# Optimization experiments

Hardware: AMD Instinct MI355X
Metric: run time of the kernel (lower is better)

The kernel has to match this reference:

```python
import jax, jax.numpy as jnp
import numpy as np

N_NODES = 20000
N_REL = 200
DIM = 128
N_EDGES = 200000
N_TIMES = 8


def setup_inputs() -> dict:
    key = jax.random.key(0)
    ks = jax.random.split(key, 12)
    s = 1.0 / np.sqrt(DIM)
    return {
        "edge_index": jax.random.randint(ks[0], (2, N_EDGES), 0, N_NODES),
        "edge_type": jax.random.randint(ks[1], (N_EDGES,), 0, N_REL),
        "edge_time": jax.random.randint(ks[2], (N_EDGES,), 0, N_TIMES),
        "edge_weight": jax.random.uniform(ks[3], (N_EDGES,), dtype=jnp.float32),
        "node_emb": jax.random.normal(ks[4], (N_NODES, DIM), dtype=jnp.float32),
        "rel_emb": jax.random.normal(ks[5], (N_REL, DIM), dtype=jnp.float32),
        "W_enc": jax.random.normal(ks[6], (DIM, DIM), dtype=jnp.float32) * s,
        "Wz": jax.random.normal(ks[7], (DIM, DIM), dtype=jnp.float32) * s,
        "Uz": jax.random.normal(ks[8], (DIM, DIM), dtype=jnp.float32) * s,
        "Wh": jax.random.normal(ks[9], (DIM, DIM), dtype=jnp.float32) * s,
        "Uh": jax.random.normal(ks[10], (DIM, DIM), dtype=jnp.float32) * s,
        "bz": jnp.zeros((DIM,), dtype=jnp.float32),
        "bh": jnp.zeros((DIM,), dtype=jnp.float32),
        "num_times": N_TIMES,
    }


def reference(edge_index, edge_type, edge_time, edge_weight,
              node_emb, rel_emb, W_enc, Wz, Uz, Wh, Uh, bz, bh, num_times):
    # TemporalEncoder.forward: loop over sorted unique timestamps; per-step
    # masked-edge GNN encode (R-GCN lite) then gated SSM cell; state detached.
    src, dst = edge_index[0], edge_index[1]
    rel_e = rel_emb[edge_type]          # [E, D] gather (constant across steps)
    src_e = node_emb[src]               # [E, D]
    n_nodes = node_emb.shape[0]

    def step(state, t):
        m = (edge_time == t).astype(edge_weight.dtype)       # [E]
        msg = src_e * rel_e * (edge_weight * m)[:, None]     # [E, D]
        agg = jax.ops.segment_sum(msg, dst, num_segments=n_nodes)  # [N, D]
        h = jnp.tanh(agg @ W_enc)                            # base_encoder output
        z = jax.nn.sigmoid(h @ Wz + state @ Uz + bz)
        cand = jnp.tanh(h @ Wh + state @ Uh + bh)
        new_state = (1.0 - z) * state + z * cand             # ssm.cell
        return jax.lax.stop_gradient(new_state), new_state   # state.detach()

    state0 = jnp.zeros_like(node_emb)
    _, outs = jax.lax.scan(step, state0, jnp.arange(num_times))
    return outs[-1]  # last_out, shape [N, D]
```

## Files before the change

### kernel.cpp

```cpp
#include <hip/hip_runtime.h>

#define N_NODES 20000
#define N_REL 200
#define N_EDGES 200000
#define DIM 128
#define T_STEPS 8
#define N_TILES (N_NODES / 16)
#define KEYS (N_NODES * T_STEPS)
#define SCAN_N (KEYS + 1)
#define SCAN_BLKS ((SCAN_N + 1023) / 1024)

typedef short short8 __attribute__((ext_vector_type(8)));
typedef float f32x4 __attribute__((ext_vector_type(4)));

static __device__ __forceinline__ unsigned short f2bf(float f) {
  union { float f; unsigned u; } v; v.f = f;
  unsigned r = v.u + 0x7fffu + ((v.u >> 16) & 1u);
  return (unsigned short)(r >> 16);
}
static __device__ __forceinline__ unsigned cvt_pk_bf16(float lo, float hi) {
  unsigned r;
  asm("v_cvt_pk_bf16_f32 %0, %1, %2" : "=v"(r) : "v"(lo), "v"(hi));
  return r;
}
static __device__ __forceinline__ float fast_tanh(float x) {
  float e = __expf(2.f * x);
  return 1.f - 2.f / (e + 1.f);
}
static __device__ __forceinline__ float fast_sig(float x) {
  return 1.f / (1.f + __expf(-x));
}

__global__ void repack5(const float* __restrict__ w0,
                        const float* __restrict__ w1,
                        const float* __restrict__ w2,
                        const float* __restrict__ w3,
                        const float* __restrict__ w4,
                        unsigned short* __restrict__ pack) {
  int i = blockIdx.x * blockDim.x + threadIdx.x;
  if (i >= 5 * 16384) return;
  int m = i >> 14, r = i & 16383;
  int j = r & 7, lane = (r >> 3) & 63, ks = (r >> 9) & 3, nt = (r >> 11) & 7;
  int n = nt * 16 + (lane & 15);
  int k = ks * 32 + (lane >> 4) * 8 + j;
  const float* w = (m == 0) ? w0 : (m == 1) ? w1 : (m == 2) ? w2
                 : (m == 3) ? w3 : w4;
  pack[i] = f2bf(w[k * DIM + n]);
}

__global__ void hist_k(const int* __restrict__ dst, const int* __restrict__ etime,
                       int* __restrict__ counts) {
  int i = blockIdx.x * blockDim.x + threadIdx.x;
  if (i >= N_EDGES) return;
  atomicAdd(&counts[dst[i] * T_STEPS + etime[i]], 1);
}

__global__ void scan1_k(const int* __restrict__ counts,
                        int* __restrict__ base, int* __restrict__ bsum) {
  __shared__ int ls[256];
  int tid = threadIdx.x;
  int i0 = blockIdx.x * 1024 + tid * 4;
  int v[4], ts = 0;
#pragma unroll
  for (int r = 0; r < 4; r++) {
    v[r] = (i0 + r < SCAN_N) ? counts[i0 + r] : 0;
    ts += v[r];
  }
  ls[tid] = ts; __syncthreads();
#pragma unroll
  for (int off = 1; off < 256; off <<= 1) {
    int x = (tid >= off) ? ls[tid - off] : 0;
    __syncthreads(); ls[tid] += x; __syncthreads();
  }
  int run = ls[tid] - ts;
  if (tid == 255) bsum[blockIdx.x] = ls[255];
#pragma unroll
  for (int r = 0; r < 4; r++) {
    if (i0 + r < SCAN_N) base[i0 + r] = run;
    run += v[r];
  }
}

__global__ void scan2_k(int* __restrict__ bsum) {
  __shared__ int ls[256];
  int tid = threadIdx.x;
  int v = (tid < SCAN_BLKS) ? bsum[tid] : 0;
  ls[tid] = v; __syncthreads();
#pragma unroll
  for (int off = 1; off < 256; off <<= 1) {
    int x = (tid >= off) ? ls[tid - off] : 0;
    __syncthreads(); ls[tid] += x; __syncthreads();
  }
  if (tid < SCAN_BLKS) bsum[tid] = ls[tid] - v;
}

__global__ void fill_k(const int* __restrict__ src, const int* __restrict__ dst,
                       const int* __restrict__ etype, const int* __restrict__ etime,
                       const float* __restrict__ ew,
                       const int* __restrict__ base, const int* __restrict__ bsum,
                       int* __restrict__ cursor, uint2* __restrict__ ep2) {
  int i = blockIdx.x * blockDim.x + threadIdx.x;
  if (i >= N_EDGES) return;
  int key = dst[i] * T_STEPS + etime[i];
  int pos = base[key] + bsum[key >> 10] + atomicAdd(&cursor[key], 1);
  uint2 e;
  e.x = (unsigned)src[i] | ((unsigned)etype[i] << 15);
  e.y = __float_as_uint(ew[i]);
  ep2[pos] = e;
}

__launch_bounds__(512, 4)
__global__ void fused_recur(const int* __restrict__ base,
                            const int* __restrict__ bsum,
                            const uint2* __restrict__ ep2,
                            const float* __restrict__ nemb,
                            const float* __restrict__ remb,
                            const unsigned short* __restrict__ pack,
                            const float* __restrict__ bz,
                            const float* __restrict__ bh,
                            float* __restrict__ out) {
  __shared__ unsigned short aggL[T_STEPS * 16 * 136];
  __shared__ unsigned short Hb[2][16 * 136];
  __shared__ unsigned short Sb[2][16 * 136];
  int lane = threadIdx.x & 63;
  int nt = threadIdx.x >> 6;
  int q = lane >> 4, l15 = lane & 15;
  int row0 = blockIdx.x * 16;
  int c = nt * 16 + l15;

#pragma unroll
  for (int ln = 0; ln < 2; ln++) {
    int nl = nt * 2 + ln;
    int kb = (row0 + nl) * T_STEPS;
    int prev = base[kb] + bsum[kb >> 10];
#pragma unroll
    for (int tt = 0; tt < T_STEPS; tt++) {
      int kn = kb + tt + 1;
      int e1 = base[kn] + bsum[kn >> 10];
      float ax = 0.f, ay = 0.f;
      for (int i = prev; i < e1; i++) {
        uint2 e = ep2[i];
        float w = __uint_as_float(e.y);
        int s = e.x & 0x7fff, rt = e.x >> 15;
        float2 sv = ((const float2*)(nemb + (size_t)s * DIM))[lane];
        float2 rv = ((const float2*)(remb + (size_t)rt * DIM))[lane];
        ax += sv.x * rv.x * w;
        ay += sv.y * rv.y * w;
      }
      prev = e1;
      ((unsigned*)&aggL[(tt * 16 + nl) * 136])[lane] = cvt_pk_bf16(ax, ay);
    }
  }
  __syncthreads();

  unsigned hpk[T_STEPS][2];
  {
    short8 wenc[4];
#pragma unroll
    for (int ks = 0; ks < 4; ks++)
      wenc[ks] = *(const short8*)(pack + ((nt * 4 + ks) * 64 + lane) * 8);
#pragma unroll
    for (int t = 0; t < T_STEPS; t++) {
      f32x4 acch = (f32x4){0.f, 0.f, 0.f, 0.f};
#pragma unroll
      for (int ks = 0; ks < 4; ks++) {
        short8 aA = *(const short8*)&aggL[(t * 16 + l15) * 136 + ks * 32 + q * 8];
        acch = __builtin_amdgcn_mfma_f32_16x16x32_bf16(aA, wenc[ks], acch, 0, 0, 0);
      }
      hpk[t][0] = cvt_pk_bf16(fast_tanh(acch[0]), fast_tanh(acch[1]));
      hpk[t][1] = cvt_pk_bf16(fast_tanh(acch[2]), fast_tanh(acch[3]));
    }
  }

  short8 wz[4], uz[4], wh[4], uh[4];
#pragma unroll
  for (int ks = 0; ks < 4; ks++) {
    int fo = ((nt * 4 + ks) * 64 + lane) * 8;
    wz[ks] = *(const short8*)(pack + 16384 * 1 + fo);
    uz[ks] = *(const short8*)(pack + 16384 * 2 + fo);
    wh[ks] = *(const short8*)(pack + 16384 * 3 + fo);
    uh[ks] = *(const short8*)(pack + 16384 * 4 + fo);
  }
  float bzv = bz[c];
  float bhv = bh[c];

  f32x4 stC = (f32x4){0.f, 0.f, 0.f, 0.f};

#pragma unroll
  for (int t = 0; t < T_STEPS; t++) {
    unsigned short* hB = Hb[t & 1];
    unsigned short* sB = Sb[t & 1];
    unsigned s01 = cvt_pk_bf16(stC[0], stC[1]);
    unsigned s23 = cvt_pk_bf16(stC[2], stC[3]);
    hB[(q * 4 + 0) * 136 + c] = (unsigned short)hpk[t][0];
    hB[(q * 4 + 1) * 136 + c] = (unsigned short)(hpk[t][0] >> 16);
    hB[(q * 4 + 2) * 136 + c] = (unsigned short)hpk[t][1];
    hB[(q * 4 + 3) * 136 + c] = (unsigned short)(hpk[t][1] >> 16);
    sB[(q * 4 + 0) * 136 + c] = (unsigned short)s01;
    sB[(q * 4 + 1) * 136 + c] = (unsigned short)(s01 >> 16);
    sB[(q * 4 + 2) * 136 + c] = (unsigned short)s23;
    sB[(q * 4 + 3) * 136 + c] = (unsigned short)(s23 >> 16);
    __syncthreads();

    f32x4 accz = (f32x4){bzv, bzv, bzv, bzv};
    f32x4 accc = (f32x4){bhv, bhv, bhv, bhv};
#pragma unroll
    for (int ks = 0; ks < 4; ks++) {
      short8 hA = *(const short8*)&hB[l15 * 136 + ks * 32 + q * 8];
      short8 sA = *(const short8*)&sB[l15 * 136 + ks * 32 + q * 8];
      accz = __builtin_amdgcn_mfma_f32_16x16x32_bf16(hA, wz[ks], accz, 0, 0, 0);
      accz = __builtin_amdgcn_mfma_f32_16x16x32_bf16(sA, uz[ks], accz, 0, 0, 0);
      accc = __builtin_amdgcn_mfma_f32_16x16x32_bf16(hA, wh[ks], accc, 0, 0, 0);
      accc = __builtin_amdgcn_mfma_f32_16x16x32_bf16(sA, uh[ks], accc, 0, 0, 0);
    }
#pragma unroll
    for (int r = 0; r < 4; r++) {
      float z = fast_sig(accz[r]);
      float cc = fast_tanh(accc[r]);
      stC[r] = (1.f - z) * stC[r] + z * cc;
    }
  }

#pragma unroll
  for (int r = 0; r < 4; r++)
    out[(size_t)(row0 + q * 4 + r) * DIM + c] = stC[r];
}

extern "C" void kernel_launch(void* const* d_in, const int* in_sizes, int n_in,
                              void* d_out, int out_size, void* d_ws, size_t ws_size,
                              hipStream_t stream) {
  const int* eidx  = (const int*)d_in[0];
  const int* src   = eidx;
  const int* dst   = eidx + N_EDGES;
  const int* etype = (const int*)d_in[1];
  const int* etime = (const int*)d_in[2];
  const float* ew   = (const float*)d_in[3];
  const float* nemb = (const float*)d_in[4];
  const float* remb = (const float*)d_in[5];
  const float* Wenc = (const float*)d_in[6];
  const float* Wz   = (const float*)d_in[7];
  const float* Uz   = (const float*)d_in[8];
  const float* Wh   = (const float*)d_in[9];
  const float* Uh   = (const float*)d_in[10];
  const float* bz   = (const float*)d_in[11];
  const float* bh   = (const float*)d_in[12];

  int* counts = (int*)d_ws;
  int* cursor = counts + SCAN_N;
  int* bsum   = cursor + KEYS;
  int* base   = bsum + 256;
  uint2* ep2  = (uint2*)(base + ((SCAN_N + 1) & ~1));
  unsigned short* pack = (unsigned short*)(ep2 + N_EDGES);
  float* outp = (float*)d_out;

  hipMemsetAsync(counts, 0, (size_t)(SCAN_N + KEYS) * sizeof(int), stream);
  repack5<<<(5 * 16384 + 255) / 256, 256, 0, stream>>>(Wenc, Wz, Uz, Wh, Uh, pack);
  hist_k<<<(N_EDGES + 255) / 256, 256, 0, stream>>>(dst, etime, counts);
  scan1_k<<<SCAN_BLKS, 256, 0, stream>>>(counts, base, bsum);
  scan2_k<<<1, 256, 0, stream>>>(bsum);
  fill_k<<<(N_EDGES + 255) / 256, 256, 0, stream>>>(src, dst, etype, etime, ew,
                                                    base, bsum, cursor, ep2);
  fused_recur<<<N_TILES, 512, 0, stream>>>(base, bsum, ep2, nemb, remb,
                                           pack, bz, bh, outp);
}
```

Before: 213.1 us.

## Interleave two nodes' edge lists with paired gathers and per-time register accumulators

The edge gather loop no longer walks each (node, time) segment serially. It packs the timestamp into the edge word and processes a node's whole edge range at once, accumulating into eight per-time register accumulators selected by predicate. Two nodes are interleaved and edges are taken in pairs, so more independent global gathers are in flight and the short, divergent per-segment loops go away. In exchange, register pressure is higher (32 accumulators) and the selects add ALU work at every edge.

```diff
diff --git a/kernel.cpp b/kernel.cpp
--- a/kernel.cpp
+++ b/kernel.cpp
@@ -101,13 +101,49 @@
                        int* __restrict__ cursor, uint2* __restrict__ ep2) {
   int i = blockIdx.x * blockDim.x + threadIdx.x;
   if (i >= N_EDGES) return;
-  int key = dst[i] * T_STEPS + etime[i];
+  int t = etime[i];
+  int key = dst[i] * T_STEPS + t;
   int pos = base[key] + bsum[key >> 10] + atomicAdd(&cursor[key], 1);
   uint2 e;
-  e.x = (unsigned)src[i] | ((unsigned)etype[i] << 15);
+  e.x = (unsigned)src[i] | ((unsigned)etype[i] << 15) | ((unsigned)t << 23);
   e.y = __float_as_uint(ew[i]);
   ep2[pos] = e;
 }
+
+#define EDGE_PAIR(i, AX, AY)                                                   \
+  {                                                                            \
+    uint2 ea = ep2[i];                                                         \
+    uint2 eb = ep2[(i) + 1];                                                   \
+    float wa = __uint_as_float(ea.y), wb = __uint_as_float(eb.y);              \
+    int sa = ea.x & 0x7fff, ra = (ea.x >> 15) & 0xff, ta = (ea.x >> 23) & 7;   \
+    int sb = eb.x & 0x7fff, rb = (eb.x >> 15) & 0xff, tb = (eb.x >> 23) & 7;   \
+    float2 sva = ((const float2*)(nemb + (size_t)sa * DIM))[lane];             \
+    float2 svb = ((const float2*)(nemb + (size_t)sb * DIM))[lane];             \
+    float2 rva = ((const float2*)(remb + (size_t)ra * DIM))[lane];             \
+    float2 rvb = ((const float2*)(remb + (size_t)rb * DIM))[lane];             \
+    float m0a = sva.x * rva.x * wa, m1a = sva.y * rva.y * wa;                  \
+    float m0b = svb.x * rvb.x * wb, m1b = svb.y * rvb.y * wb;                  \
+    _Pragma("unroll")                                                          \
+    for (int tt = 0; tt < T_STEPS; tt++) {                                     \
+      AX[tt] += ((ta == tt) ? m0a : 0.f) + ((tb == tt) ? m0b : 0.f);           \
+      AY[tt] += ((ta == tt) ? m1a : 0.f) + ((tb == tt) ? m1b : 0.f);           \
+    }                                                                          \
+  }
+
+#define EDGE_ONE(i, AX, AY)                                                    \
+  {                                                                            \
+    uint2 ea = ep2[i];                                                         \
+    float wa = __uint_as_float(ea.y);                                          \
+    int sa = ea.x & 0x7fff, ra = (ea.x >> 15) & 0xff, ta = (ea.x >> 23) & 7;   \
+    float2 sva = ((const float2*)(nemb + (size_t)sa * DIM))[lane];             \
+    float2 rva = ((const float2*)(remb + (size_t)ra * DIM))[lane];             \
+    float m0a = sva.x * rva.x * wa, m1a = sva.y * rva.y * wa;                  \
+    _Pragma("unroll")                                                          \
+    for (int tt = 0; tt < T_STEPS; tt++) {                                     \
+      AX[tt] += (ta == tt) ? m0a : 0.f;                                        \
+      AY[tt] += (ta == tt) ? m1a : 0.f;                                        \
+    }                                                                          \
+  }
 
 __launch_bounds__(512, 4)
 __global__ void fused_recur(const int* __restrict__ base,
@@ -125,30 +161,36 @@
   int lane = threadIdx.x & 63;
   int nt = threadIdx.x >> 6;
   int q = lane >> 4, l15 = lane & 15;
-  int row0 = blockIdx.x * 16;
+  int tile = blockIdx.x;
+  int row0 = tile * 16;
   int c = nt * 16 + l15;
 
-#pragma unroll
-  for (int ln = 0; ln < 2; ln++) {
-    int nl = nt * 2 + ln;
-    int kb = (row0 + nl) * T_STEPS;
-    int prev = base[kb] + bsum[kb >> 10];
+  {
+    int kb0 = (row0 + nt * 2) * T_STEPS;
+    int kb1 = kb0 + T_STEPS;
+    int ke1 = kb1 + T_STEPS;
+    int i0 = base[kb0] + bsum[kb0 >> 10];
+    int e0 = base[kb1] + bsum[kb1 >> 10];
+    int i1 = e0;
+    int e1 = base[ke1] + bsum[ke1 >> 10];
+
+    float ax0[T_STEPS], ay0[T_STEPS], ax1[T_STEPS], ay1[T_STEPS];
 #pragma unroll
     for (int tt = 0; tt < T_STEPS; tt++) {
-      int kn = kb + tt + 1;
-      int e1 = base[kn] + bsum[kn >> 10];
-      float ax = 0.f, ay = 0.f;
-      for (int i = prev; i < e1; i++) {
-        uint2 e = ep2[i];
-        float w = __uint_as_float(e.y);
-        int s = e.x & 0x7fff, rt = e.x >> 15;
-        float2 sv = ((const float2*)(nemb + (size_t)s * DIM))[lane];
-        float2 rv = ((const float2*)(remb + (size_t)rt * DIM))[lane];
-        ax += sv.x * rv.x * w;
-        ay += sv.y * rv.y * w;
-      }
-      prev = e1;
-      ((unsigned*)&aggL[(tt * 16 + nl) * 136])[lane] = cvt_pk_bf16(ax, ay);
+      ax0[tt] = 0.f; ay0[tt] = 0.f; ax1[tt] = 0.f; ay1[tt] = 0.f;
+    }
+
+    while (i0 + 1 < e0 || i1 + 1 < e1) {
+      if (i0 + 1 < e0) { EDGE_PAIR(i0, ax0, ay0); i0 += 2; }
+      if (i1 + 1 < e1) { EDGE_PAIR(i1, ax1, ay1); i1 += 2; }
+    }
+    if (i0 < e0) EDGE_ONE(i0, ax0, ay0);
+    if (i1 < e1) EDGE_ONE(i1, ax1, ay1);
+
+#pragma unroll
+    for (int tt = 0; tt < T_STEPS; tt++) {
+      ((unsigned*)&aggL[(tt * 16 + nt * 2 + 0) * 136])[lane] = cvt_pk_bf16(ax0[tt], ay0[tt]);
+      ((unsigned*)&aggL[(tt * 16 + nt * 2 + 1) * 136])[lane] = cvt_pk_bf16(ax1[tt], ay1[tt]);
     }
   }
   __syncthreads();
```

Result: faster. 196.6 us (-7.7%).

## Interleave two nodes' edge gathers with time-tagged edges and register accumulators

Applied to the files above, without the earlier changes.

The fill kernel now packs each edge's timestep into spare bits of the packed index word. The gather phase no longer runs a serial loop per (node, timestep) segment. It walks all edges of two nodes at once, loading two edges per node per iteration, and routes each message into one of eight register accumulators by a switch on the embedded timestep. This is meant to expose more independent memory loads per wave and remove the short-loop overhead of eight tiny segments. In exchange it raises register pressure, adds branchy switch code, and performs masked dummy loads at segment ends.

```diff
diff --git a/kernel.cpp b/kernel.cpp
--- a/kernel.cpp
+++ b/kernel.cpp
@@ -101,13 +101,55 @@
                        int* __restrict__ cursor, uint2* __restrict__ ep2) {
   int i = blockIdx.x * blockDim.x + threadIdx.x;
   if (i >= N_EDGES) return;
-  int key = dst[i] * T_STEPS + etime[i];
+  int t = etime[i];
+  int key = dst[i] * T_STEPS + t;
   int pos = base[key] + bsum[key >> 10] + atomicAdd(&cursor[key], 1);
   uint2 e;
-  e.x = (unsigned)src[i] | ((unsigned)etype[i] << 15);
+  e.x = (unsigned)src[i] | ((unsigned)etype[i] << 15) | ((unsigned)t << 23);
   e.y = __float_as_uint(ew[i]);
   ep2[pos] = e;
 }
+
+#define EDGE_LOAD(jj, valid, M0, M1, TT)                                      \
+  int TT; float M0, M1;                                                       \
+  {                                                                           \
+    int j_ = (jj) < (N_EDGES - 1) ? (jj) : (N_EDGES - 1);                     \
+    uint2 e_ = ep2[j_];                                                       \
+    unsigned x_ = (unsigned)__builtin_amdgcn_readfirstlane((int)e_.x);        \
+    float w_ = __uint_as_float(                                               \
+        (unsigned)__builtin_amdgcn_readfirstlane((int)e_.y));                 \
+    w_ = (valid) ? w_ : 0.f;                                                  \
+    int s_ = (int)(x_ & 0x7fffu), r_ = (int)((x_ >> 15) & 0xffu);             \
+    TT = (int)((x_ >> 23) & 7u);                                              \
+    float2 sv_ = *(const float2*)(nemb + (size_t)s_ * DIM + 2 * lane);        \
+    float2 rv_ = *(const float2*)(remb + (size_t)r_ * DIM + 2 * lane);        \
+    M0 = sv_.x * rv_.x * w_;                                                  \
+    M1 = sv_.y * rv_.y * w_;                                                  \
+  }
+
+#define ACC_SWITCH(TT, AXP, AYP, M0, M1)                                      \
+  switch (TT) {                                                               \
+    case 0: AXP##0 += M0; AYP##0 += M1; break;                                \
+    case 1: AXP##1 += M0; AYP##1 += M1; break;                                \
+    case 2: AXP##2 += M0; AYP##2 += M1; break;                                \
+    case 3: AXP##3 += M0; AYP##3 += M1; break;                                \
+    case 4: AXP##4 += M0; AYP##4 += M1; break;                                \
+    case 5: AXP##5 += M0; AYP##5 += M1; break;                                \
+    case 6: AXP##6 += M0; AYP##6 += M1; break;                                \
+    default: AXP##7 += M0; AYP##7 += M1; break;                               \
+  }
+
+#define DECL8(P) float P##0 = 0.f, P##1 = 0.f, P##2 = 0.f, P##3 = 0.f,        \
+                       P##4 = 0.f, P##5 = 0.f, P##6 = 0.f, P##7 = 0.f
+
+#define STROW(TT, NL, AX, AY)                                                 \
+  ((unsigned*)&aggL[((TT) * 16 + (NL)) * 136])[lane] = cvt_pk_bf16(AX, AY)
+
+#define STROW8(NL, AXP, AYP)                                                  \
+  STROW(0, NL, AXP##0, AYP##0); STROW(1, NL, AXP##1, AYP##1);                 \
+  STROW(2, NL, AXP##2, AYP##2); STROW(3, NL, AXP##3, AYP##3);                 \
+  STROW(4, NL, AXP##4, AYP##4); STROW(5, NL, AXP##5, AYP##5);                 \
+  STROW(6, NL, AXP##6, AYP##6); STROW(7, NL, AXP##7, AYP##7)
 
 __launch_bounds__(512, 4)
 __global__ void fused_recur(const int* __restrict__ base,
@@ -125,31 +167,39 @@
   int lane = threadIdx.x & 63;
   int nt = threadIdx.x >> 6;
   int q = lane >> 4, l15 = lane & 15;
-  int row0 = blockIdx.x * 16;
+  int tile = blockIdx.x;
+  int row0 = tile * 16;
   int c = nt * 16 + l15;
 
-#pragma unroll
-  for (int ln = 0; ln < 2; ln++) {
-    int nl = nt * 2 + ln;
-    int kb = (row0 + nl) * T_STEPS;
-    int prev = base[kb] + bsum[kb >> 10];
-#pragma unroll
-    for (int tt = 0; tt < T_STEPS; tt++) {
-      int kn = kb + tt + 1;
-      int e1 = base[kn] + bsum[kn >> 10];
-      float ax = 0.f, ay = 0.f;
-      for (int i = prev; i < e1; i++) {
-        uint2 e = ep2[i];
-        float w = __uint_as_float(e.y);
-        int s = e.x & 0x7fff, rt = e.x >> 15;
-        float2 sv = ((const float2*)(nemb + (size_t)s * DIM))[lane];
-        float2 rv = ((const float2*)(remb + (size_t)rt * DIM))[lane];
-        ax += sv.x * rv.x * w;
-        ay += sv.y * rv.y * w;
-      }
-      prev = e1;
-      ((unsigned*)&aggL[(tt * 16 + nl) * 136])[lane] = cvt_pk_bf16(ax, ay);
+  {
+    int kb0 = (row0 + nt * 2) * T_STEPS;
+    int kb1 = kb0 + T_STEPS;
+    int ke1 = kb1 + T_STEPS;
+    int i0 = __builtin_amdgcn_readfirstlane(base[kb0] + bsum[kb0 >> 10]);
+    int e0 = __builtin_amdgcn_readfirstlane(base[kb1] + bsum[kb1 >> 10]);
+    int i1 = e0;
+    int e1 = __builtin_amdgcn_readfirstlane(base[ke1] + bsum[ke1 >> 10]);
+
+    DECL8(ax0_); DECL8(ay0_); DECL8(ax1_); DECL8(ay1_);
+
+    while (i0 < e0 || i1 < e1) {
+      bool vA0 = i0 < e0,     vB0 = i0 + 1 < e0;
+      bool vA1 = i1 < e1,     vB1 = i1 + 1 < e1;
+      EDGE_LOAD(i0,     vA0, m0A0, m1A0, tA0);
+      EDGE_LOAD(i0 + 1, vB0, m0B0, m1B0, tB0);
+      EDGE_LOAD(i1,     vA1, m0A1, m1A1, tA1);
+      EDGE_LOAD(i1 + 1, vB1, m0B1, m1B1, tB1);
+      ACC_SWITCH(tA0, ax0_, ay0_, m0A0, m1A0);
+      ACC_SWITCH(tB0, ax0_, ay0_, m0B0, m1B0);
+      ACC_SWITCH(tA1, ax1_, ay1_, m0A1, m1A1);
+      ACC_SWITCH(tB1, ax1_, ay1_, m0B1, m1B1);
+      i0 = (i0 + 2 < e0) ? i0 + 2 : e0;
+      i1 = (i1 + 2 < e1) ? i1 + 2 : e1;
     }
+
+    int nl0 = nt * 2, nl1 = nt * 2 + 1;
+    STROW8(nl0, ax0_, ay0_);
+    STROW8(nl1, ax1_, ay1_);
   }
   __syncthreads();
 
```

Result: faster. 192.3 us (-9.8%).
